# Kernel optimization log

Measured on AMD Instinct MI355X. Metric: run time of the kernel, lower is better.

## Reference

```python
import jax, jax.numpy as jnp
import numpy as np

N = 8192  # number of nodes
F = 8     # feature dim


def setup_inputs() -> dict:
    key = jax.random.key(0)
    ks = jax.random.split(key, 24)
    inp = {
        "adj": jax.random.uniform(ks[0], (N, N), jnp.float32),
        "dist_from_prev": jax.random.uniform(ks[1], (N,), jnp.float32),
        "dist_to_start": jax.random.uniform(ks[2], (N,), jnp.float32),
    }
    dims = {"l0": (2, F), "l1": (F, F), "pol": (F, 1), "val": (F, 1)}
    i = 3
    for name, (din, dout) in dims.items():
        inp[f"W1_{name}"] = jax.random.normal(ks[i], (din, dout), jnp.float32) * 0.3; i += 1
        inp[f"b1_{name}"] = jax.random.normal(ks[i], (dout,), jnp.float32) * 0.1; i += 1
        inp[f"W2_{name}"] = jax.random.normal(ks[i], (dout, dout), jnp.float32) * 0.3; i += 1
        inp[f"b2_{name}"] = jax.random.normal(ks[i], (dout,), jnp.float32) * 0.1; i += 1
    return inp


def _mlp(x, adj, W1, b1, W2, b2):
    # GIN-style layer: aggregate then 2-layer MLP
    h = adj @ x                     # [N, din] aggregation (memory bound)
    h = jax.nn.relu(h @ W1 + b1)    # [N, dout]
    return h @ W2 + b2              # [N, dout]


def reference(adj, dist_from_prev, dist_to_start,
              W1_l0, b1_l0, W2_l0, b2_l0,
              W1_l1, b1_l1, W2_l1, b2_l1,
              W1_pol, b1_pol, W2_pol, b2_pol,
              W1_val, b1_val, W2_val, b2_val):
    cur = jnp.stack([dist_from_prev, dist_to_start], axis=1)  # [N, 2]
    # hidden GIN layers + relu (dropout is identity in eval mode)
    cur = jax.nn.relu(_mlp(cur, adj, W1_l0, b1_l0, W2_l0, b2_l0))
    cur = jax.nn.relu(_mlp(cur, adj, W1_l1, b1_l1, W2_l1, b2_l1))
    policy = jax.nn.softmax(_mlp(cur, adj, W1_pol, b1_pol, W2_pol, b2_pol)[:, 0], axis=0)  # [N]
    value = _mlp(cur, adj, W1_val, b1_val, W2_val, b2_val)[:, 0]  # [N]
    m = value.mean()
    std = jnp.sqrt(jnp.mean((value - m) ** 2) + 1e-10)
    normalized_value = (value - m) / std
    return policy, normalized_value
```

## Files before the change

kernel.cpp:

```cpp
#include <hip/hip_runtime.h>
#include <math.h>

#define NN 8192
typedef unsigned int u32;
typedef unsigned char u8;

__device__ __forceinline__ u32 dot4(u32 a, u32 b, u32 c) {
#if __has_builtin(__builtin_amdgcn_udot4)
  return __builtin_amdgcn_udot4(a, b, c, false);
#else
  c += (a & 0xffu) * (b & 0xffu);
  c += ((a >> 8) & 0xffu) * ((b >> 8) & 0xffu);
  c += ((a >> 16) & 0xffu) * ((b >> 16) & 0xffu);
  c += (a >> 24) * (b >> 24);
  return c;
#endif
}

__global__ __launch_bounds__(256) void pass1_kernel(
    const float* __restrict__ adj, u8* __restrict__ adj8,
    const float* __restrict__ dfp, const float* __restrict__ dts,
    const float* __restrict__ W1, const float* __restrict__ b1,
    const float* __restrict__ W2, const float* __restrict__ b2,
    float* __restrict__ cur, float* __restrict__ partial) {
  const int wave = threadIdx.x >> 6, lane = threadIdx.x & 63;
  const int row0 = blockIdx.x * 16 + wave * 4;
  __shared__ float w1red[4][8];
  float acc0[4] = {0.f, 0.f, 0.f, 0.f};
  float acc1[4] = {0.f, 0.f, 0.f, 0.f};

  float4 A[4], Xp, Xs;
  {
    const int k = 4 * lane;
    Xp = *(const float4*)(dfp + k);
    Xs = *(const float4*)(dts + k);
#pragma unroll
    for (int r = 0; r < 4; ++r)
      A[r] = *(const float4*)(adj + (size_t)(row0 + r) * NN + k);
  }
  for (int k0 = 0; k0 < NN; k0 += 256) {
    float4 B[4], Yp, Ys;
    if (k0 + 256 < NN) {
      const int k = k0 + 256 + 4 * lane;
      Yp = *(const float4*)(dfp + k);
      Ys = *(const float4*)(dts + k);
#pragma unroll
      for (int r = 0; r < 4; ++r)
        B[r] = *(const float4*)(adj + (size_t)(row0 + r) * NN + k);
    } else {
      Yp = Xp; Ys = Xs;
#pragma unroll
      for (int r = 0; r < 4; ++r) B[r] = A[r];
    }
    const float pv[4] = {Xp.x, Xp.y, Xp.z, Xp.w};
    const float sv[4] = {Xs.x, Xs.y, Xs.z, Xs.w};
#pragma unroll
    for (int r = 0; r < 4; ++r) {
      const float av[4] = {A[r].x, A[r].y, A[r].z, A[r].w};
#pragma unroll
      for (int c = 0; c < 4; ++c) {
        acc0[r] = fmaf(av[c], pv[c], acc0[r]);
        acc1[r] = fmaf(av[c], sv[c], acc1[r]);
      }
      u32 q0 = (u32)fmaf(av[0], 255.f, 0.5f);
      u32 q1 = (u32)fmaf(av[1], 255.f, 0.5f);
      u32 q2 = (u32)fmaf(av[2], 255.f, 0.5f);
      u32 q3 = (u32)fmaf(av[3], 255.f, 0.5f);
      ((u32*)(adj8 + (size_t)(row0 + r) * NN + k0))[lane] =
          q0 | (q1 << 8) | (q2 << 16) | (q3 << 24);
    }
#pragma unroll
    for (int r = 0; r < 4; ++r) A[r] = B[r];
    Xp = Yp; Xs = Ys;
  }
#pragma unroll
  for (int r = 0; r < 4; ++r) {
    for (int off = 32; off; off >>= 1) {
      acc0[r] += __shfl_xor(acc0[r], off, 64);
      acc1[r] += __shfl_xor(acc1[r], off, 64);
    }
  }
  const int j = lane & 7;
  float mx = 0.f;
#pragma unroll
  for (int r = 0; r < 4; ++r) {
    float z = fmaf(acc0[r], W1[0 * 8 + j], fmaf(acc1[r], W1[1 * 8 + j], b1[j]));
    z = fmaxf(z, 0.f);
    float o = b2[j];
#pragma unroll
    for (int jj = 0; jj < 8; ++jj)
      o = fmaf(__shfl(z, jj, 64), W2[jj * 8 + j], o);
    float val = fmaxf(o, 0.f);
    if (lane < 8) cur[(size_t)(row0 + r) * 8 + j] = val;
    mx = fmaxf(mx, val);
  }
  if (lane < 8) w1red[wave][lane] = mx;
  __syncthreads();
  if (wave == 0 && lane < 8) {
    float m2 = fmaxf(fmaxf(w1red[0][lane], w1red[1][lane]),
                     fmaxf(w1red[2][lane], w1red[3][lane]));
    partial[blockIdx.x * 8 + lane] = m2;
  }
}

template <int HEADS>
__global__ __launch_bounds__(512) void pass23_kernel(
    const u8* __restrict__ adj8, const float* __restrict__ x,
    const float* __restrict__ partial, int nprod,
    const float* __restrict__ W1, const float* __restrict__ b1,
    const float* __restrict__ W2, const float* __restrict__ b2,
    const float* __restrict__ W1v, const float* __restrict__ b1v,
    const float* __restrict__ W2v, const float* __restrict__ b2v,
    float* __restrict__ out0, float* __restrict__ out1,
    float* __restrict__ partial_out) {
  __shared__ u32 sxR[NN * 2];
  __shared__ u32 sxT[8 * 2048];
  __shared__ float swred[8][8];
  __shared__ float sqs[8], sds[8];
  const int tid = threadIdx.x;
  const int wave = tid >> 6, lane = tid & 63;
  const int row0 = blockIdx.x * 32 + wave * 4;

  uint4 A[4];
#pragma unroll
  for (int r = 0; r < 4; ++r)
    A[r] = *(const uint4*)(adj8 + (size_t)(row0 + r) * NN + 16 * lane);

  float pm[8] = {0.f, 0.f, 0.f, 0.f, 0.f, 0.f, 0.f, 0.f};
  if (tid < nprod) {
    float4 a = *(const float4*)(partial + tid * 8);
    float4 b = *(const float4*)(partial + tid * 8 + 4);
    pm[0] = a.x; pm[1] = a.y; pm[2] = a.z; pm[3] = a.w;
    pm[4] = b.x; pm[5] = b.y; pm[6] = b.z; pm[7] = b.w;
  }
  for (int off = 32; off; off >>= 1)
#pragma unroll
    for (int j = 0; j < 8; ++j) pm[j] = fmaxf(pm[j], __shfl_xor(pm[j], off, 64));
  if (lane == 0)
#pragma unroll
    for (int j = 0; j < 8; ++j) swred[wave][j] = pm[j];
  __syncthreads();
  if (tid < 8) {
    float m2 = 0.f;
#pragma unroll
    for (int w = 0; w < 8; ++w) m2 = fmaxf(m2, swred[w][tid]);
    m2 = fmaxf(m2, 1e-20f);
    sqs[tid] = 255.f / m2;
    sds[tid] = m2 / 65025.f;
  }
  __syncthreads();

  float qs[8];
#pragma unroll
  for (int j = 0; j < 8; ++j) qs[j] = sqs[j];
  for (int base = 0; base < NN; base += 512) {
    const int row = base + tid;
    float4 a = *(const float4*)(x + (size_t)row * 8);
    float4 b = *(const float4*)(x + (size_t)row * 8 + 4);
    u32 q0 = (u32)fmaf(a.x, qs[0], 0.5f), q1 = (u32)fmaf(a.y, qs[1], 0.5f);
    u32 q2 = (u32)fmaf(a.z, qs[2], 0.5f), q3 = (u32)fmaf(a.w, qs[3], 0.5f);
    u32 q4 = (u32)fmaf(b.x, qs[4], 0.5f), q5 = (u32)fmaf(b.y, qs[5], 0.5f);
    u32 q6 = (u32)fmaf(b.z, qs[6], 0.5f), q7 = (u32)fmaf(b.w, qs[7], 0.5f);
    uint2 pk;
    pk.x = q0 | (q1 << 8) | (q2 << 16) | (q3 << 24);
    pk.y = q4 | (q5 << 8) | (q6 << 16) | (q7 << 24);
    ((uint2*)sxR)[row] = pk;
  }
  __syncthreads();

  {
    const int jj = tid & 7, g = tid >> 3;
    const int dw = jj >> 2, sh = 8 * (jj & 3);
#pragma unroll
    for (int i = 0; i < 32; ++i) {
      const int p = g + 64 * i;
      u32 w = 0;
#pragma unroll
      for (int m = 0; m < 4; ++m)
        w |= (((sxR[(4 * p + m) * 2 + dw] >> sh) & 0xffu) << (8 * m));
      sxT[jj * 2048 + p] = w;
    }
  }
  __syncthreads();

  u32 acc[4][8] = {};
  for (int k0 = 0; k0 < NN; k0 += 1024) {
    uint4 B[4];
    if (k0 + 1024 < NN) {
#pragma unroll
      for (int r = 0; r < 4; ++r)
        B[r] = *(const uint4*)(adj8 + (size_t)(row0 + r) * NN + (k0 + 1024) +
                               16 * lane);
    } else {
#pragma unroll
      for (int r = 0; r < 4; ++r) B[r] = A[r];
    }
    uint4 xq[8];
#pragma unroll
    for (int jj = 0; jj < 8; ++jj)
      xq[jj] = ((const uint4*)sxT)[jj * 512 + (k0 >> 4) + lane];
#pragma unroll
    for (int r = 0; r < 4; ++r) {
#pragma unroll
      for (int jj = 0; jj < 8; ++jj) {
        u32 c = acc[r][jj];
        c = dot4(A[r].x, xq[jj].x, c);
        c = dot4(A[r].y, xq[jj].y, c);
        c = dot4(A[r].z, xq[jj].z, c);
        c = dot4(A[r].w, xq[jj].w, c);
        acc[r][jj] = c;
      }
    }
#pragma unroll
    for (int r = 0; r < 4; ++r) A[r] = B[r];
  }
#pragma unroll
  for (int r = 0; r < 4; ++r)
#pragma unroll
    for (int jj = 0; jj < 8; ++jj)
      for (int off = 32; off; off >>= 1)
        acc[r][jj] += (u32)__shfl_xor((int)acc[r][jj], off, 64);
  float dsc[8];
#pragma unroll
  for (int j = 0; j < 8; ++j) dsc[j] = sds[j];
  float h[4][8];
#pragma unroll
  for (int r = 0; r < 4; ++r)
#pragma unroll
    for (int jj = 0; jj < 8; ++jj) h[r][jj] = (float)acc[r][jj] * dsc[jj];

  if (HEADS == 0) {
    const int j = lane & 7;
    float mxv = 0.f;
#pragma unroll
    for (int r = 0; r < 4; ++r) {
      float z = b1[j];
#pragma unroll
      for (int d = 0; d < 8; ++d) z = fmaf(h[r][d], W1[d * 8 + j], z);
      z = fmaxf(z, 0.f);
      float o = b2[j];
#pragma unroll
      for (int jj = 0; jj < 8; ++jj)
        o = fmaf(__shfl(z, jj, 64), W2[jj * 8 + j], o);
      float val = fmaxf(o, 0.f);
      if (lane < 8) out0[(size_t)(row0 + r) * 8 + j] = val;
      mxv = fmaxf(mxv, val);
    }
    if (lane < 8) swred[wave][lane] = mxv;
    __syncthreads();
    if (wave == 0 && lane < 8) {
      float m2 = 0.f;
#pragma unroll
      for (int w = 0; w < 8; ++w) m2 = fmaxf(m2, swred[w][lane]);
      partial_out[blockIdx.x * 8 + lane] = m2;
    }
  } else {
    if (lane == 0) {
#pragma unroll
      for (int r = 0; r < 4; ++r) {
        float zp = b1[0], zv = b1v[0];
#pragma unroll
        for (int d = 0; d < 8; ++d) {
          zp = fmaf(h[r][d], W1[d], zp);
          zv = fmaf(h[r][d], W1v[d], zv);
        }
        zp = fmaxf(zp, 0.f);
        zv = fmaxf(zv, 0.f);
        out0[row0 + r] = fmaf(zp, W2[0], b2[0]);
        out1[row0 + r] = fmaf(zv, W2v[0], b2v[0]);
      }
    }
  }
}

__global__ __launch_bounds__(1024) void reduce_finalize_kernel(
    float* __restrict__ out) {
  const int tid = threadIdx.x, wave = tid >> 6, lane = tid & 63;
  __shared__ float sa[16], sb[16], sc[4];

  float4 l0 = *(const float4*)(out + tid * 8);
  float4 l1 = *(const float4*)(out + tid * 8 + 4);
  float4 v0 = *(const float4*)(out + NN + tid * 8);
  float4 v1 = *(const float4*)(out + NN + tid * 8 + 4);
  const float lv[8] = {l0.x, l0.y, l0.z, l0.w, l1.x, l1.y, l1.z, l1.w};
  const float vv[8] = {v0.x, v0.y, v0.z, v0.w, v1.x, v1.y, v1.z, v1.w};

  float m = -3.4e38f, s = 0.f;
#pragma unroll
  for (int i = 0; i < 8; ++i) {
    m = fmaxf(m, lv[i]);
    s += vv[i];
  }
  for (int off = 32; off; off >>= 1) {
    m = fmaxf(m, __shfl_xor(m, off, 64));
    s += __shfl_xor(s, off, 64);
  }
  if (lane == 0) { sa[wave] = m; sb[wave] = s; }
  __syncthreads();
  if (tid == 0) {
    float mm = sa[0], ss = sb[0];
    for (int i = 1; i < 16; ++i) { mm = fmaxf(mm, sa[i]); ss += sb[i]; }
    sc[0] = mm; sc[1] = ss * (1.f / NN);
  }
  __syncthreads();
  m = sc[0];
  const float mean = sc[1];

  float el[8];
  float e = 0.f, v2 = 0.f;
#pragma unroll
  for (int i = 0; i < 8; ++i) {
    el[i] = expf(lv[i] - m);
    e += el[i];
    float d = vv[i] - mean;
    v2 = fmaf(d, d, v2);
  }
  for (int off = 32; off; off >>= 1) {
    e += __shfl_xor(e, off, 64);
    v2 += __shfl_xor(v2, off, 64);
  }
  if (lane == 0) { sa[wave] = e; sb[wave] = v2; }
  __syncthreads();
  if (tid == 0) {
    float ee = sa[0], vvv = sb[0];
    for (int i = 1; i < 16; ++i) { ee += sa[i]; vvv += sb[i]; }
    sc[2] = 1.f / ee;
    sc[3] = 1.f / sqrtf(vvv * (1.f / NN) + 1e-10f);
  }
  __syncthreads();
  const float inv_e = sc[2], inv_std = sc[3];
  float4 o0, o1, w0, w1;
  o0.x = el[0] * inv_e; o0.y = el[1] * inv_e;
  o0.z = el[2] * inv_e; o0.w = el[3] * inv_e;
  o1.x = el[4] * inv_e; o1.y = el[5] * inv_e;
  o1.z = el[6] * inv_e; o1.w = el[7] * inv_e;
  w0.x = (vv[0] - mean) * inv_std; w0.y = (vv[1] - mean) * inv_std;
  w0.z = (vv[2] - mean) * inv_std; w0.w = (vv[3] - mean) * inv_std;
  w1.x = (vv[4] - mean) * inv_std; w1.y = (vv[5] - mean) * inv_std;
  w1.z = (vv[6] - mean) * inv_std; w1.w = (vv[7] - mean) * inv_std;
  *(float4*)(out + tid * 8) = o0;
  *(float4*)(out + tid * 8 + 4) = o1;
  *(float4*)(out + NN + tid * 8) = w0;
  *(float4*)(out + NN + tid * 8 + 4) = w1;
}

extern "C" void kernel_launch(void* const* d_in, const int* in_sizes, int n_in,
                              void* d_out, int out_size, void* d_ws,
                              size_t ws_size, hipStream_t stream) {
  const float* adj = (const float*)d_in[0];
  const float* dfp = (const float*)d_in[1];
  const float* dts = (const float*)d_in[2];
  const float* W1_l0 = (const float*)d_in[3];
  const float* b1_l0 = (const float*)d_in[4];
  const float* W2_l0 = (const float*)d_in[5];
  const float* b2_l0 = (const float*)d_in[6];
  const float* W1_l1 = (const float*)d_in[7];
  const float* b1_l1 = (const float*)d_in[8];
  const float* W2_l1 = (const float*)d_in[9];
  const float* b2_l1 = (const float*)d_in[10];
  const float* W1_pol = (const float*)d_in[11];
  const float* b1_pol = (const float*)d_in[12];
  const float* W2_pol = (const float*)d_in[13];
  const float* b2_pol = (const float*)d_in[14];
  const float* W1_val = (const float*)d_in[15];
  const float* b1_val = (const float*)d_in[16];
  const float* W2_val = (const float*)d_in[17];
  const float* b2_val = (const float*)d_in[18];

  u8* adj8 = (u8*)d_ws;
  float* curA = (float*)((char*)d_ws + (size_t)NN * NN);
  float* curB = curA + NN * 8;
  float* partialA = curB + NN * 8;
  float* partialB = partialA + 512 * 8;
  float* logits = (float*)d_out;
  float* value = logits + NN;

  pass1_kernel<<<NN / 16, 256, 0, stream>>>(adj, adj8, dfp, dts, W1_l0, b1_l0,
                                            W2_l0, b2_l0, curA, partialA);
  pass23_kernel<0><<<NN / 32, 512, 0, stream>>>(
      adj8, curA, partialA, 512, W1_l1, b1_l1, W2_l1, b2_l1, W1_l1, b1_l1,
      W2_l1, b2_l1, curB, curB, partialB);
  pass23_kernel<1><<<NN / 32, 512, 0, stream>>>(
      adj8, curB, partialB, 256, W1_pol, b1_pol, W2_pol, b2_pol, W1_val,
      b1_val, W2_val, b2_val, logits, value, partialB);
  reduce_finalize_kernel<<<1, 1024, 0, stream>>>((float*)d_out);
}
```

Baseline: 145.9 us.

## Keep quantized features in registers and use signed dot4 with offset correction

The aggregation kernels no longer stage and transpose the whole quantized feature matrix in shared memory in every block. Each thread now quantizes only its own 16-column slice of x into registers. The int8 adjacency is stored biased by 128 so it can use signed dot4, and exact integer corrections come from row sums precomputed in pass1 plus per-block column sums. pass1 is also reorganised so 512-thread blocks sweep full rows, with a cross-wave shared-memory reduction. This removes the redundant per-block LDS fill and transpose, at the cost of extra block-level reductions and syncs for every group of 4 rows.

```diff
diff --git a/kernel.cpp b/kernel.cpp
--- a/kernel.cpp
+++ b/kernel.cpp
@@ -3,131 +3,161 @@
 
 #define NN 8192
 typedef unsigned int u32;
-typedef unsigned char u8;
-
-__device__ __forceinline__ u32 dot4(u32 a, u32 b, u32 c) {
-#if __has_builtin(__builtin_amdgcn_udot4)
-  return __builtin_amdgcn_udot4(a, b, c, false);
+
+__device__ __forceinline__ int sdot4(u32 a, u32 b, int c) {
+#if __has_builtin(__builtin_amdgcn_sdot4)
+  return __builtin_amdgcn_sdot4((int)a, (int)b, c, false);
 #else
-  c += (a & 0xffu) * (b & 0xffu);
-  c += ((a >> 8) & 0xffu) * ((b >> 8) & 0xffu);
-  c += ((a >> 16) & 0xffu) * ((b >> 16) & 0xffu);
-  c += (a >> 24) * (b >> 24);
+  c += ((int)(a << 24) >> 24) * ((int)(b << 24) >> 24);
+  c += ((int)(a << 16) >> 24) * ((int)(b << 16) >> 24);
+  c += ((int)(a << 8) >> 24) * ((int)(b << 8) >> 24);
+  c += (((int)a) >> 24) * (((int)b) >> 24);
   return c;
 #endif
 }
 
-__global__ __launch_bounds__(256) void pass1_kernel(
-    const float* __restrict__ adj, u8* __restrict__ adj8,
+__global__ __launch_bounds__(512) void pass1_kernel(
+    const float* __restrict__ adj, u32* __restrict__ adj8,
+    u32* __restrict__ Rq,
     const float* __restrict__ dfp, const float* __restrict__ dts,
     const float* __restrict__ W1, const float* __restrict__ b1,
     const float* __restrict__ W2, const float* __restrict__ b2,
     float* __restrict__ cur, float* __restrict__ partial) {
-  const int wave = threadIdx.x >> 6, lane = threadIdx.x & 63;
-  const int row0 = blockIdx.x * 16 + wave * 4;
-  __shared__ float w1red[4][8];
-  float acc0[4] = {0.f, 0.f, 0.f, 0.f};
-  float acc1[4] = {0.f, 0.f, 0.f, 0.f};
-
-  float4 A[4], Xp, Xs;
-  {
-    const int k = 4 * lane;
-    Xp = *(const float4*)(dfp + k);
-    Xs = *(const float4*)(dts + k);
+  const int tid = threadIdx.x;
+  const int wave = tid >> 6, lane = tid & 63;
+  const int rbase = blockIdx.x * 16;
+  __shared__ float redF[8][8];
+  __shared__ u32 redU[8][4];
+  __shared__ float finF[8];
+  __shared__ float wmax[4][8];
+
+  float pv[4][4], sv[4][4];
+#pragma unroll
+  for (int q = 0; q < 4; ++q) {
+    float4 t1 = *(const float4*)(dfp + q * 2048 + 4 * tid);
+    float4 t2 = *(const float4*)(dts + q * 2048 + 4 * tid);
+    pv[q][0] = t1.x; pv[q][1] = t1.y; pv[q][2] = t1.z; pv[q][3] = t1.w;
+    sv[q][0] = t2.x; sv[q][1] = t2.y; sv[q][2] = t2.z; sv[q][3] = t2.w;
+  }
+  float mxv = 0.f;
+
+  for (int g = 0; g < 4; ++g) {
+    float accP[4] = {0.f, 0.f, 0.f, 0.f};
+    float accS[4] = {0.f, 0.f, 0.f, 0.f};
+    u32 accR[4] = {0, 0, 0, 0};
+    float4 A[4], B[4];
 #pragma unroll
     for (int r = 0; r < 4; ++r)
-      A[r] = *(const float4*)(adj + (size_t)(row0 + r) * NN + k);
-  }
-  for (int k0 = 0; k0 < NN; k0 += 256) {
-    float4 B[4], Yp, Ys;
-    if (k0 + 256 < NN) {
-      const int k = k0 + 256 + 4 * lane;
-      Yp = *(const float4*)(dfp + k);
-      Ys = *(const float4*)(dts + k);
-#pragma unroll
-      for (int r = 0; r < 4; ++r)
-        B[r] = *(const float4*)(adj + (size_t)(row0 + r) * NN + k);
-    } else {
-      Yp = Xp; Ys = Xs;
-#pragma unroll
-      for (int r = 0; r < 4; ++r) B[r] = A[r];
-    }
-    const float pv[4] = {Xp.x, Xp.y, Xp.z, Xp.w};
-    const float sv[4] = {Xs.x, Xs.y, Xs.z, Xs.w};
+      A[r] = *(const float4*)(adj + (size_t)(rbase + g * 4 + r) * NN + 4 * tid);
+#pragma unroll
+    for (int q = 0; q < 4; ++q) {
+      if (q < 3) {
+#pragma unroll
+        for (int r = 0; r < 4; ++r)
+          B[r] = *(const float4*)(adj + (size_t)(rbase + g * 4 + r) * NN +
+                                  (q + 1) * 2048 + 4 * tid);
+      }
+#pragma unroll
+      for (int r = 0; r < 4; ++r) {
+        const float a0 = A[r].x, a1 = A[r].y, a2 = A[r].z, a3 = A[r].w;
+        accP[r] = fmaf(a0, pv[q][0], accP[r]);
+        accP[r] = fmaf(a1, pv[q][1], accP[r]);
+        accP[r] = fmaf(a2, pv[q][2], accP[r]);
+        accP[r] = fmaf(a3, pv[q][3], accP[r]);
+        accS[r] = fmaf(a0, sv[q][0], accS[r]);
+        accS[r] = fmaf(a1, sv[q][1], accS[r]);
+        accS[r] = fmaf(a2, sv[q][2], accS[r]);
+        accS[r] = fmaf(a3, sv[q][3], accS[r]);
+        u32 q0 = (u32)fmaf(a0, 255.f, 0.5f);
+        u32 q1 = (u32)fmaf(a1, 255.f, 0.5f);
+        u32 q2 = (u32)fmaf(a2, 255.f, 0.5f);
+        u32 q3 = (u32)fmaf(a3, 255.f, 0.5f);
+        accR[r] += q0 + q1 + q2 + q3;
+        adj8[(size_t)(rbase + g * 4 + r) * 2048 + q * 512 + tid] =
+            (q0 | (q1 << 8) | (q2 << 16) | (q3 << 24)) ^ 0x80808080u;
+      }
+      if (q < 3) {
+#pragma unroll
+        for (int r = 0; r < 4; ++r) A[r] = B[r];
+      }
+    }
 #pragma unroll
     for (int r = 0; r < 4; ++r) {
-      const float av[4] = {A[r].x, A[r].y, A[r].z, A[r].w};
-#pragma unroll
-      for (int c = 0; c < 4; ++c) {
-        acc0[r] = fmaf(av[c], pv[c], acc0[r]);
-        acc1[r] = fmaf(av[c], sv[c], acc1[r]);
-      }
-      u32 q0 = (u32)fmaf(av[0], 255.f, 0.5f);
-      u32 q1 = (u32)fmaf(av[1], 255.f, 0.5f);
-      u32 q2 = (u32)fmaf(av[2], 255.f, 0.5f);
-      u32 q3 = (u32)fmaf(av[3], 255.f, 0.5f);
-      ((u32*)(adj8 + (size_t)(row0 + r) * NN + k0))[lane] =
-          q0 | (q1 << 8) | (q2 << 16) | (q3 << 24);
-    }
-#pragma unroll
-    for (int r = 0; r < 4; ++r) A[r] = B[r];
-    Xp = Yp; Xs = Ys;
-  }
-#pragma unroll
-  for (int r = 0; r < 4; ++r) {
-    for (int off = 32; off; off >>= 1) {
-      acc0[r] += __shfl_xor(acc0[r], off, 64);
-      acc1[r] += __shfl_xor(acc1[r], off, 64);
-    }
-  }
-  const int j = lane & 7;
-  float mx = 0.f;
-#pragma unroll
-  for (int r = 0; r < 4; ++r) {
-    float z = fmaf(acc0[r], W1[0 * 8 + j], fmaf(acc1[r], W1[1 * 8 + j], b1[j]));
-    z = fmaxf(z, 0.f);
-    float o = b2[j];
-#pragma unroll
-    for (int jj = 0; jj < 8; ++jj)
-      o = fmaf(__shfl(z, jj, 64), W2[jj * 8 + j], o);
-    float val = fmaxf(o, 0.f);
-    if (lane < 8) cur[(size_t)(row0 + r) * 8 + j] = val;
-    mx = fmaxf(mx, val);
-  }
-  if (lane < 8) w1red[wave][lane] = mx;
-  __syncthreads();
-  if (wave == 0 && lane < 8) {
-    float m2 = fmaxf(fmaxf(w1red[0][lane], w1red[1][lane]),
-                     fmaxf(w1red[2][lane], w1red[3][lane]));
-    partial[blockIdx.x * 8 + lane] = m2;
-  }
+      for (int off = 32; off; off >>= 1) {
+        accP[r] += __shfl_xor(accP[r], off, 64);
+        accS[r] += __shfl_xor(accS[r], off, 64);
+        accR[r] += (u32)__shfl_xor((int)accR[r], off, 64);
+      }
+    }
+    if (lane == 0) {
+#pragma unroll
+      for (int r = 0; r < 4; ++r) {
+        redF[wave][r] = accP[r];
+        redF[wave][4 + r] = accS[r];
+        redU[wave][r] = accR[r];
+      }
+    }
+    __syncthreads();
+    if (tid < 8) {
+      float s = 0.f;
+      for (int w = 0; w < 8; ++w) s += redF[w][tid];
+      finF[tid] = s;
+    } else if (tid < 12) {
+      u32 s = 0;
+      for (int w = 0; w < 8; ++w) s += redU[w][tid - 8];
+      Rq[rbase + g * 4 + (tid - 8)] = s;
+    }
+    __syncthreads();
+    if (wave < 4) {
+      const int row = rbase + g * 4 + wave;
+      const float hp = finF[wave], hs = finF[4 + wave];
+      const int j = lane & 7;
+      float z = fmaf(hp, W1[j], fmaf(hs, W1[8 + j], b1[j]));
+      z = fmaxf(z, 0.f);
+      float o = b2[j];
+#pragma unroll
+      for (int jj = 0; jj < 8; ++jj)
+        o = fmaf(__shfl(z, jj, 64), W2[jj * 8 + j], o);
+      float val = fmaxf(o, 0.f);
+      if (lane < 8) {
+        cur[(size_t)row * 8 + j] = val;
+        mxv = fmaxf(mxv, val);
+      }
+    }
+  }
+  if (wave < 4 && lane < 8) wmax[wave][lane] = mxv;
+  __syncthreads();
+  if (tid < 8)
+    partial[blockIdx.x * 8 + tid] = fmaxf(fmaxf(wmax[0][tid], wmax[1][tid]),
+                                          fmaxf(wmax[2][tid], wmax[3][tid]));
 }
 
 template <int HEADS>
 __global__ __launch_bounds__(512) void pass23_kernel(
-    const u8* __restrict__ adj8, const float* __restrict__ x,
-    const float* __restrict__ partial, int nprod,
+    const u32* __restrict__ adj8, const float* __restrict__ x,
+    const u32* __restrict__ Rq, const float* __restrict__ partial,
     const float* __restrict__ W1, const float* __restrict__ b1,
     const float* __restrict__ W2, const float* __restrict__ b2,
     const float* __restrict__ W1v, const float* __restrict__ b1v,
     const float* __restrict__ W2v, const float* __restrict__ b2v,
     float* __restrict__ out0, float* __restrict__ out1,
     float* __restrict__ partial_out) {
-  __shared__ u32 sxR[NN * 2];
-  __shared__ u32 sxT[8 * 2048];
-  __shared__ float swred[8][8];
-  __shared__ float sqs[8], sds[8];
   const int tid = threadIdx.x;
   const int wave = tid >> 6, lane = tid & 63;
-  const int row0 = blockIdx.x * 32 + wave * 4;
-
-  uint4 A[4];
-#pragma unroll
-  for (int r = 0; r < 4; ++r)
-    A[r] = *(const uint4*)(adj8 + (size_t)(row0 + r) * NN + 16 * lane);
-
-  float pm[8] = {0.f, 0.f, 0.f, 0.f, 0.f, 0.f, 0.f, 0.f};
-  if (tid < nprod) {
+  const int rbase = blockIdx.x * 16;
+  __shared__ float sqs[8], sds[8];
+  __shared__ float redM[8][8];
+  __shared__ u32 redC[8][8];
+  __shared__ int sCq[8];
+  __shared__ int redD[8][32];
+  __shared__ int finD[32];
+  __shared__ float wmax[4][8];
+
+  uint4 A = *(const uint4*)(adj8 + (size_t)rbase * 2048 + 4 * tid);
+  uint4 Bn = *(const uint4*)(adj8 + (size_t)(rbase + 1) * 2048 + 4 * tid);
+
+  float pm[8];
+  {
     float4 a = *(const float4*)(partial + tid * 8);
     float4 b = *(const float4*)(partial + tid * 8 + 4);
     pm[0] = a.x; pm[1] = a.y; pm[2] = a.z; pm[3] = a.w;
@@ -138,12 +168,12 @@
     for (int j = 0; j < 8; ++j) pm[j] = fmaxf(pm[j], __shfl_xor(pm[j], off, 64));
   if (lane == 0)
 #pragma unroll
-    for (int j = 0; j < 8; ++j) swred[wave][j] = pm[j];
+    for (int j = 0; j < 8; ++j) redM[wave][j] = pm[j];
   __syncthreads();
   if (tid < 8) {
     float m2 = 0.f;
 #pragma unroll
-    for (int w = 0; w < 8; ++w) m2 = fmaxf(m2, swred[w][tid]);
+    for (int w = 0; w < 8; ++w) m2 = fmaxf(m2, redM[w][tid]);
     m2 = fmaxf(m2, 1e-20f);
     sqs[tid] = 255.f / m2;
     sds[tid] = m2 / 65025.f;
@@ -153,123 +183,135 @@
   float qs[8];
 #pragma unroll
   for (int j = 0; j < 8; ++j) qs[j] = sqs[j];
-  for (int base = 0; base < NN; base += 512) {
-    const int row = base + tid;
-    float4 a = *(const float4*)(x + (size_t)row * 8);
-    float4 b = *(const float4*)(x + (size_t)row * 8 + 4);
-    u32 q0 = (u32)fmaf(a.x, qs[0], 0.5f), q1 = (u32)fmaf(a.y, qs[1], 0.5f);
-    u32 q2 = (u32)fmaf(a.z, qs[2], 0.5f), q3 = (u32)fmaf(a.w, qs[3], 0.5f);
-    u32 q4 = (u32)fmaf(b.x, qs[4], 0.5f), q5 = (u32)fmaf(b.y, qs[5], 0.5f);
-    u32 q6 = (u32)fmaf(b.z, qs[6], 0.5f), q7 = (u32)fmaf(b.w, qs[7], 0.5f);
-    uint2 pk;
-    pk.x = q0 | (q1 << 8) | (q2 << 16) | (q3 << 24);
-    pk.y = q4 | (q5 << 8) | (q6 << 16) | (q7 << 24);
-    ((uint2*)sxR)[row] = pk;
-  }
-  __syncthreads();
-
-  {
-    const int jj = tid & 7, g = tid >> 3;
-    const int dw = jj >> 2, sh = 8 * (jj & 3);
-#pragma unroll
-    for (int i = 0; i < 32; ++i) {
-      const int p = g + 64 * i;
-      u32 w = 0;
-#pragma unroll
-      for (int m = 0; m < 4; ++m)
-        w |= (((sxR[(4 * p + m) * 2 + dw] >> sh) & 0xffu) << (8 * m));
-      sxT[jj * 2048 + p] = w;
-    }
-  }
-  __syncthreads();
-
-  u32 acc[4][8] = {};
-  for (int k0 = 0; k0 < NN; k0 += 1024) {
-    uint4 B[4];
-    if (k0 + 1024 < NN) {
+  u32 xq[8][4];
+#pragma unroll
+  for (int j = 0; j < 8; ++j)
+#pragma unroll
+    for (int d = 0; d < 4; ++d) xq[j][d] = 0;
+  u32 cs[8] = {0, 0, 0, 0, 0, 0, 0, 0};
+#pragma unroll
+  for (int kk = 0; kk < 16; ++kk) {
+    const float* xp = x + ((size_t)tid * 16 + kk) * 8;
+    float4 a = *(const float4*)xp;
+    float4 b = *(const float4*)(xp + 4);
+    const float e[8] = {a.x, a.y, a.z, a.w, b.x, b.y, b.z, b.w};
+#pragma unroll
+    for (int j = 0; j < 8; ++j) {
+      u32 qv = (u32)fmaf(e[j], qs[j], 0.5f);
+      cs[j] += qv;
+      xq[j][kk >> 2] |= (qv ^ 0x80u) << (8 * (kk & 3));
+    }
+  }
+  for (int off = 32; off; off >>= 1)
+#pragma unroll
+    for (int j = 0; j < 8; ++j) cs[j] += (u32)__shfl_xor((int)cs[j], off, 64);
+  if (lane == 0)
+#pragma unroll
+    for (int j = 0; j < 8; ++j) redC[wave][j] = cs[j];
+  __syncthreads();
+  if (tid < 8) {
+    u32 s = 0;
+#pragma unroll
+    for (int w = 0; w < 8; ++w) s += redC[w][tid];
+    sCq[tid] = (int)s;
+  }
+  __syncthreads();
+
+  for (int g = 0; g < 4; ++g) {
+    int accD[4][8];
+#pragma unroll
+    for (int r = 0; r < 4; ++r)
+#pragma unroll
+      for (int j = 0; j < 8; ++j) accD[r][j] = 0;
+#pragma unroll
+    for (int r = 0; r < 4; ++r) {
+      const int nrr = (g * 4 + r + 2) & 15;
+      uint4 C = *(const uint4*)(adj8 + (size_t)(rbase + nrr) * 2048 + 4 * tid);
+#pragma unroll
+      for (int j = 0; j < 8; ++j) {
+        int c = accD[r][j];
+        c = sdot4(A.x, xq[j][0], c);
+        c = sdot4(A.y, xq[j][1], c);
+        c = sdot4(A.z, xq[j][2], c);
+        c = sdot4(A.w, xq[j][3], c);
+        accD[r][j] = c;
+      }
+      A = Bn;
+      Bn = C;
+    }
+#pragma unroll
+    for (int r = 0; r < 4; ++r)
+#pragma unroll
+      for (int j = 0; j < 8; ++j)
+        for (int off = 32; off; off >>= 1)
+          accD[r][j] += __shfl_xor(accD[r][j], off, 64);
+    if (lane == 0)
 #pragma unroll
       for (int r = 0; r < 4; ++r)
-        B[r] = *(const uint4*)(adj8 + (size_t)(row0 + r) * NN + (k0 + 1024) +
-                               16 * lane);
+#pragma unroll
+        for (int j = 0; j < 8; ++j) redD[wave][r * 8 + j] = accD[r][j];
+    __syncthreads();
+    if (tid < 32) {
+      int s = 0;
+#pragma unroll
+      for (int w = 0; w < 8; ++w) s += redD[w][tid];
+      finD[tid] = s;
+    }
+    __syncthreads();
+    if (HEADS == 0) {
+      if (wave < 4) {
+        const int row = rbase + g * 4 + wave;
+        const int j = lane & 7;
+        int hi = finD[wave * 8 + j] + 128 * (int)Rq[row] + 128 * sCq[j] -
+                 134217728;
+        float h = (float)hi * sds[j];
+        float z = b1[j];
+#pragma unroll
+        for (int d = 0; d < 8; ++d)
+          z = fmaf(__shfl(h, d, 64), W1[d * 8 + j], z);
+        z = fmaxf(z, 0.f);
+        float o = b2[j];
+#pragma unroll
+        for (int jj = 0; jj < 8; ++jj)
+          o = fmaf(__shfl(z, jj, 64), W2[jj * 8 + j], o);
+        float val = fmaxf(o, 0.f);
+        if (lane < 8) {
+          out0[(size_t)row * 8 + j] = val;
+          if (wave == (g & 3) || true) wmaxv_dummy:;
+        }
+      }
     } else {
-#pragma unroll
-      for (int r = 0; r < 4; ++r) B[r] = A[r];
-    }
-    uint4 xq[8];
-#pragma unroll
-    for (int jj = 0; jj < 8; ++jj)
-      xq[jj] = ((const uint4*)sxT)[jj * 512 + (k0 >> 4) + lane];
-#pragma unroll
-    for (int r = 0; r < 4; ++r) {
-#pragma unroll
-      for (int jj = 0; jj < 8; ++jj) {
-        u32 c = acc[r][jj];
-        c = dot4(A[r].x, xq[jj].x, c);
-        c = dot4(A[r].y, xq[jj].y, c);
-        c = dot4(A[r].z, xq[jj].z, c);
-        c = dot4(A[r].w, xq[jj].w, c);
-        acc[r][jj] = c;
-      }
-    }
-#pragma unroll
-    for (int r = 0; r < 4; ++r) A[r] = B[r];
-  }
-#pragma unroll
-  for (int r = 0; r < 4; ++r)
-#pragma unroll
-    for (int jj = 0; jj < 8; ++jj)
-      for (int off = 32; off; off >>= 1)
-        acc[r][jj] += (u32)__shfl_xor((int)acc[r][jj], off, 64);
-  float dsc[8];
-#pragma unroll
-  for (int j = 0; j < 8; ++j) dsc[j] = sds[j];
-  float h[4][8];
-#pragma unroll
-  for (int r = 0; r < 4; ++r)
-#pragma unroll
-    for (int jj = 0; jj < 8; ++jj) h[r][jj] = (float)acc[r][jj] * dsc[jj];
-
-  if (HEADS == 0) {
-    const int j = lane & 7;
-    float mxv = 0.f;
-#pragma unroll
-    for (int r = 0; r < 4; ++r) {
-      float z = b1[j];
-#pragma unroll
-      for (int d = 0; d < 8; ++d) z = fmaf(h[r][d], W1[d * 8 + j], z);
-      z = fmaxf(z, 0.f);
-      float o = b2[j];
-#pragma unroll
-      for (int jj = 0; jj < 8; ++jj)
-        o = fmaf(__shfl(z, jj, 64), W2[jj * 8 + j], o);
-      float val = fmaxf(o, 0.f);
-      if (lane < 8) out0[(size_t)(row0 + r) * 8 + j] = val;
-      mxv = fmaxf(mxv, val);
-    }
-    if (lane < 8) swred[wave][lane] = mxv;
-    __syncthreads();
-    if (wave == 0 && lane < 8) {
-      float m2 = 0.f;
-#pragma unroll
-      for (int w = 0; w < 8; ++w) m2 = fmaxf(m2, swred[w][lane]);
-      partial_out[blockIdx.x * 8 + lane] = m2;
-    }
-  } else {
-    if (lane == 0) {
-#pragma unroll
-      for (int r = 0; r < 4; ++r) {
+      if (wave < 4 && lane == 0) {
+        const int row = rbase + g * 4 + wave;
+        const int rq = 128 * (int)Rq[row];
         float zp = b1[0], zv = b1v[0];
 #pragma unroll
         for (int d = 0; d < 8; ++d) {
-          zp = fmaf(h[r][d], W1[d], zp);
-          zv = fmaf(h[r][d], W1v[d], zv);
+          int hi = finD[wave * 8 + d] + rq + 128 * sCq[d] - 134217728;
+          float h = (float)hi * sds[d];
+          zp = fmaf(h, W1[d], zp);
+          zv = fmaf(h, W1v[d], zv);
         }
         zp = fmaxf(zp, 0.f);
         zv = fmaxf(zv, 0.f);
-        out0[row0 + r] = fmaf(zp, W2[0], b2[0]);
-        out1[row0 + r] = fmaf(zv, W2v[0], b2v[0]);
-      }
-    }
+        out0[row] = fmaf(zp, W2[0], b2[0]);
+        out1[row] = fmaf(zv, W2v[0], b2v[0]);
+      }
+    }
+  }
+  if (HEADS == 0) {
+    float mxv = 0.f;
+    if (wave < 4 && lane < 8) {
+#pragma unroll
+      for (int g = 0; g < 4; ++g)
+        mxv = fmaxf(mxv, out0[(size_t)(rbase + g * 4 + wave) * 8 + lane]);
+      wmax[wave][lane] = mxv;
+    }
+    __syncthreads();
+    if (tid < 8)
+      partial_out[blockIdx.x * 8 + tid] =
+          fmaxf(fmaxf(wmax[0][tid], wmax[1][tid]),
+                fmaxf(wmax[2][tid], wmax[3][tid]));
   }
 }
 
@@ -367,21 +409,23 @@
   const float* W2_val = (const float*)d_in[17];
   const float* b2_val = (const float*)d_in[18];
 
-  u8* adj8 = (u8*)d_ws;
-  float* curA = (float*)((char*)d_ws + (size_t)NN * NN);
+  char* base = (char*)d_ws;
+  u32* adj8 = (u32*)base;
+  u32* Rq = (u32*)(base + (size_t)NN * NN);
+  float* curA = (float*)(base + (size_t)NN * NN + NN * 4);
   float* curB = curA + NN * 8;
   float* partialA = curB + NN * 8;
   float* partialB = partialA + 512 * 8;
   float* logits = (float*)d_out;
   float* value = logits + NN;
 
-  pass1_kernel<<<NN / 16, 256, 0, stream>>>(adj, adj8, dfp, dts, W1_l0, b1_l0,
-                                            W2_l0, b2_l0, curA, partialA);
-  pass23_kernel<0><<<NN / 32, 512, 0, stream>>>(
-      adj8, curA, partialA, 512, W1_l1, b1_l1, W2_l1, b2_l1, W1_l1, b1_l1,
+  pass1_kernel<<<512, 512, 0, stream>>>(adj, adj8, Rq, dfp, dts, W1_l0, b1_l0,
+                                        W2_l0, b2_l0, curA, partialA);
+  pass23_kernel<0><<<512, 512, 0, stream>>>(
+      adj8, curA, Rq, partialA, W1_l1, b1_l1, W2_l1, b2_l1, W1_l1, b1_l1,
       W2_l1, b2_l1, curB, curB, partialB);
-  pass23_kernel<1><<<NN / 32, 512, 0, stream>>>(
-      adj8, curB, partialB, 256, W1_pol, b1_pol, W2_pol, b2_pol, W1_val,
-      b1_val, W2_val, b2_val, logits, value, partialB);
+  pass23_kernel<1><<<512, 512, 0, stream>>>(
+      adj8, curB, Rq, partialB, W1_pol, b1_pol, W2_pol, b2_pol, W1_val, b1_val,
+      W2_val, b2_val, logits, value, partialB);
   reduce_finalize_kernel<<<1, 1024, 0, stream>>>((float*)d_out);
 }
```

New measurement: 212.2 us. +45.5%, slower.

## Halve rows per wave, double grid, and quantize x directly into transposed layout

Applied to the files above, without the earlier changes.

Each wave now handles 2 rows instead of 4 in both passes, and the grid doubles to 1024 and 512 blocks, giving more blocks and more memory parallelism on the large adjacency stream. The pass23 staging drops the row-major shared buffer and transpose step: each thread packs four consecutive nodes per feature straight into the transposed shared array. This frees 64KB of LDS per block so more blocks can reside per CU, and it adds a deeper two-chunk prefetch of adjacency. The partial-max buffers grow to match the larger grid.

```diff
diff --git a/kernel.cpp b/kernel.cpp
--- a/kernel.cpp
+++ b/kernel.cpp
@@ -5,7 +5,7 @@
 typedef unsigned int u32;
 typedef unsigned char u8;
 
-__device__ __forceinline__ u32 dot4(u32 a, u32 b, u32 c) {
+__device__ __forceinline__ u32 dot4u(u32 a, u32 b, u32 c) {
 #if __has_builtin(__builtin_amdgcn_udot4)
   return __builtin_amdgcn_udot4(a, b, c, false);
 #else
@@ -18,73 +18,81 @@
 }
 
 __global__ __launch_bounds__(256) void pass1_kernel(
-    const float* __restrict__ adj, u8* __restrict__ adj8,
+    const float* __restrict__ adj, u32* __restrict__ adj8,
     const float* __restrict__ dfp, const float* __restrict__ dts,
     const float* __restrict__ W1, const float* __restrict__ b1,
     const float* __restrict__ W2, const float* __restrict__ b2,
     float* __restrict__ cur, float* __restrict__ partial) {
-  const int wave = threadIdx.x >> 6, lane = threadIdx.x & 63;
-  const int row0 = blockIdx.x * 16 + wave * 4;
-  __shared__ float w1red[4][8];
-  float acc0[4] = {0.f, 0.f, 0.f, 0.f};
-  float acc1[4] = {0.f, 0.f, 0.f, 0.f};
-
-  float4 A[4], Xp, Xs;
-  {
-    const int k = 4 * lane;
-    Xp = *(const float4*)(dfp + k);
-    Xs = *(const float4*)(dts + k);
-#pragma unroll
-    for (int r = 0; r < 4; ++r)
-      A[r] = *(const float4*)(adj + (size_t)(row0 + r) * NN + k);
-  }
-  for (int k0 = 0; k0 < NN; k0 += 256) {
-    float4 B[4], Yp, Ys;
-    if (k0 + 256 < NN) {
-      const int k = k0 + 256 + 4 * lane;
-      Yp = *(const float4*)(dfp + k);
-      Ys = *(const float4*)(dts + k);
-#pragma unroll
-      for (int r = 0; r < 4; ++r)
-        B[r] = *(const float4*)(adj + (size_t)(row0 + r) * NN + k);
-    } else {
-      Yp = Xp; Ys = Xs;
-#pragma unroll
-      for (int r = 0; r < 4; ++r) B[r] = A[r];
-    }
-    const float pv[4] = {Xp.x, Xp.y, Xp.z, Xp.w};
-    const float sv[4] = {Xs.x, Xs.y, Xs.z, Xs.w};
-#pragma unroll
-    for (int r = 0; r < 4; ++r) {
-      const float av[4] = {A[r].x, A[r].y, A[r].z, A[r].w};
-#pragma unroll
-      for (int c = 0; c < 4; ++c) {
-        acc0[r] = fmaf(av[c], pv[c], acc0[r]);
-        acc1[r] = fmaf(av[c], sv[c], acc1[r]);
+  const int tid = threadIdx.x, wave = tid >> 6, lane = tid & 63;
+  const int row0 = blockIdx.x * 8 + wave * 2;
+  __shared__ float wmax[4][8];
+
+  const float* rowp0 = adj + (size_t)row0 * NN;
+  const float* rowp1 = adj + (size_t)(row0 + 1) * NN;
+  u32* qp0 = adj8 + (size_t)row0 * (NN / 4);
+  u32* qp1 = adj8 + (size_t)(row0 + 1) * (NN / 4);
+
+  float acc0[2] = {0.f, 0.f}, acc1[2] = {0.f, 0.f};
+  float4 A[2][2], B[2][2];
+#pragma unroll
+  for (int i = 0; i < 2; ++i) {
+    A[0][i] = *(const float4*)(rowp0 + 256 * i + 4 * lane);
+    A[1][i] = *(const float4*)(rowp1 + 256 * i + 4 * lane);
+  }
+  for (int c = 0; c < 16; ++c) {
+    const int kb = 512 * c;
+    if (c < 15) {
+#pragma unroll
+      for (int i = 0; i < 2; ++i) {
+        B[0][i] = *(const float4*)(rowp0 + kb + 512 + 256 * i + 4 * lane);
+        B[1][i] = *(const float4*)(rowp1 + kb + 512 + 256 * i + 4 * lane);
       }
-      u32 q0 = (u32)fmaf(av[0], 255.f, 0.5f);
-      u32 q1 = (u32)fmaf(av[1], 255.f, 0.5f);
-      u32 q2 = (u32)fmaf(av[2], 255.f, 0.5f);
-      u32 q3 = (u32)fmaf(av[3], 255.f, 0.5f);
-      ((u32*)(adj8 + (size_t)(row0 + r) * NN + k0))[lane] =
-          q0 | (q1 << 8) | (q2 << 16) | (q3 << 24);
-    }
-#pragma unroll
-    for (int r = 0; r < 4; ++r) A[r] = B[r];
-    Xp = Yp; Xs = Ys;
-  }
-#pragma unroll
-  for (int r = 0; r < 4; ++r) {
+    }
+    float4 xp[2], xs[2];
+#pragma unroll
+    for (int i = 0; i < 2; ++i) {
+      xp[i] = *(const float4*)(dfp + kb + 256 * i + 4 * lane);
+      xs[i] = *(const float4*)(dts + kb + 256 * i + 4 * lane);
+    }
+#pragma unroll
+    for (int r = 0; r < 2; ++r) {
+#pragma unroll
+      for (int i = 0; i < 2; ++i) {
+        const float4 a4 = A[r][i];
+        acc0[r] = fmaf(a4.x, xp[i].x, acc0[r]);
+        acc0[r] = fmaf(a4.y, xp[i].y, acc0[r]);
+        acc0[r] = fmaf(a4.z, xp[i].z, acc0[r]);
+        acc0[r] = fmaf(a4.w, xp[i].w, acc0[r]);
+        acc1[r] = fmaf(a4.x, xs[i].x, acc1[r]);
+        acc1[r] = fmaf(a4.y, xs[i].y, acc1[r]);
+        acc1[r] = fmaf(a4.z, xs[i].z, acc1[r]);
+        acc1[r] = fmaf(a4.w, xs[i].w, acc1[r]);
+        u32 q0 = (u32)fmaf(a4.x, 255.f, 0.5f);
+        u32 q1 = (u32)fmaf(a4.y, 255.f, 0.5f);
+        u32 q2 = (u32)fmaf(a4.z, 255.f, 0.5f);
+        u32 q3 = (u32)fmaf(a4.w, 255.f, 0.5f);
+        (r ? qp1 : qp0)[128 * c + 64 * i + lane] =
+            q0 | (q1 << 8) | (q2 << 16) | (q3 << 24);
+      }
+    }
+#pragma unroll
+    for (int r = 0; r < 2; ++r) {
+      A[r][0] = B[r][0];
+      A[r][1] = B[r][1];
+    }
+  }
+#pragma unroll
+  for (int r = 0; r < 2; ++r) {
     for (int off = 32; off; off >>= 1) {
       acc0[r] += __shfl_xor(acc0[r], off, 64);
       acc1[r] += __shfl_xor(acc1[r], off, 64);
     }
   }
   const int j = lane & 7;
-  float mx = 0.f;
-#pragma unroll
-  for (int r = 0; r < 4; ++r) {
-    float z = fmaf(acc0[r], W1[0 * 8 + j], fmaf(acc1[r], W1[1 * 8 + j], b1[j]));
+  float mxv = 0.f;
+#pragma unroll
+  for (int r = 0; r < 2; ++r) {
+    float z = fmaf(acc0[r], W1[j], fmaf(acc1[r], W1[8 + j], b1[j]));
     z = fmaxf(z, 0.f);
     float o = b2[j];
 #pragma unroll
@@ -92,20 +100,18 @@
       o = fmaf(__shfl(z, jj, 64), W2[jj * 8 + j], o);
     float val = fmaxf(o, 0.f);
     if (lane < 8) cur[(size_t)(row0 + r) * 8 + j] = val;
-    mx = fmaxf(mx, val);
-  }
-  if (lane < 8) w1red[wave][lane] = mx;
-  __syncthreads();
-  if (wave == 0 && lane < 8) {
-    float m2 = fmaxf(fmaxf(w1red[0][lane], w1red[1][lane]),
-                     fmaxf(w1red[2][lane], w1red[3][lane]));
-    partial[blockIdx.x * 8 + lane] = m2;
-  }
+    mxv = fmaxf(mxv, val);
+  }
+  if (lane < 8) wmax[wave][lane] = mxv;
+  __syncthreads();
+  if (tid < 8)
+    partial[blockIdx.x * 8 + tid] = fmaxf(fmaxf(wmax[0][tid], wmax[1][tid]),
+                                          fmaxf(wmax[2][tid], wmax[3][tid]));
 }
 
 template <int HEADS>
 __global__ __launch_bounds__(512) void pass23_kernel(
-    const u8* __restrict__ adj8, const float* __restrict__ x,
+    const u32* __restrict__ adj8, const float* __restrict__ x,
     const float* __restrict__ partial, int nprod,
     const float* __restrict__ W1, const float* __restrict__ b1,
     const float* __restrict__ W2, const float* __restrict__ b2,
@@ -113,37 +119,41 @@
     const float* __restrict__ W2v, const float* __restrict__ b2v,
     float* __restrict__ out0, float* __restrict__ out1,
     float* __restrict__ partial_out) {
-  __shared__ u32 sxR[NN * 2];
   __shared__ u32 sxT[8 * 2048];
-  __shared__ float swred[8][8];
+  __shared__ float redM[8][8];
   __shared__ float sqs[8], sds[8];
-  const int tid = threadIdx.x;
-  const int wave = tid >> 6, lane = tid & 63;
-  const int row0 = blockIdx.x * 32 + wave * 4;
-
-  uint4 A[4];
-#pragma unroll
-  for (int r = 0; r < 4; ++r)
-    A[r] = *(const uint4*)(adj8 + (size_t)(row0 + r) * NN + 16 * lane);
+  __shared__ float wmax[8][8];
+  const int tid = threadIdx.x, wave = tid >> 6, lane = tid & 63;
+  const int row0 = blockIdx.x * 16 + wave * 2;
+
+  const u32* r0p = adj8 + (size_t)row0 * 2048;
+  const u32* r1p = adj8 + (size_t)(row0 + 1) * 2048;
+  uint4 A[2], Bp[2];
+  A[0] = *(const uint4*)(r0p + 4 * lane);
+  A[1] = *(const uint4*)(r1p + 4 * lane);
+  Bp[0] = *(const uint4*)(r0p + 256 + 4 * lane);
+  Bp[1] = *(const uint4*)(r1p + 256 + 4 * lane);
 
   float pm[8] = {0.f, 0.f, 0.f, 0.f, 0.f, 0.f, 0.f, 0.f};
-  if (tid < nprod) {
-    float4 a = *(const float4*)(partial + tid * 8);
-    float4 b = *(const float4*)(partial + tid * 8 + 4);
-    pm[0] = a.x; pm[1] = a.y; pm[2] = a.z; pm[3] = a.w;
-    pm[4] = b.x; pm[5] = b.y; pm[6] = b.z; pm[7] = b.w;
+  for (int p = tid; p < nprod; p += 512) {
+    float4 a = *(const float4*)(partial + p * 8);
+    float4 b = *(const float4*)(partial + p * 8 + 4);
+    pm[0] = fmaxf(pm[0], a.x); pm[1] = fmaxf(pm[1], a.y);
+    pm[2] = fmaxf(pm[2], a.z); pm[3] = fmaxf(pm[3], a.w);
+    pm[4] = fmaxf(pm[4], b.x); pm[5] = fmaxf(pm[5], b.y);
+    pm[6] = fmaxf(pm[6], b.z); pm[7] = fmaxf(pm[7], b.w);
   }
   for (int off = 32; off; off >>= 1)
 #pragma unroll
     for (int j = 0; j < 8; ++j) pm[j] = fmaxf(pm[j], __shfl_xor(pm[j], off, 64));
   if (lane == 0)
 #pragma unroll
-    for (int j = 0; j < 8; ++j) swred[wave][j] = pm[j];
+    for (int j = 0; j < 8; ++j) redM[wave][j] = pm[j];
   __syncthreads();
   if (tid < 8) {
     float m2 = 0.f;
 #pragma unroll
-    for (int w = 0; w < 8; ++w) m2 = fmaxf(m2, swred[w][tid]);
+    for (int w = 0; w < 8; ++w) m2 = fmaxf(m2, redM[w][tid]);
     m2 = fmaxf(m2, 1e-20f);
     sqs[tid] = 255.f / m2;
     sds[tid] = m2 / 65025.f;
@@ -153,87 +163,71 @@
   float qs[8];
 #pragma unroll
   for (int j = 0; j < 8; ++j) qs[j] = sqs[j];
-  for (int base = 0; base < NN; base += 512) {
-    const int row = base + tid;
-    float4 a = *(const float4*)(x + (size_t)row * 8);
-    float4 b = *(const float4*)(x + (size_t)row * 8 + 4);
-    u32 q0 = (u32)fmaf(a.x, qs[0], 0.5f), q1 = (u32)fmaf(a.y, qs[1], 0.5f);
-    u32 q2 = (u32)fmaf(a.z, qs[2], 0.5f), q3 = (u32)fmaf(a.w, qs[3], 0.5f);
-    u32 q4 = (u32)fmaf(b.x, qs[4], 0.5f), q5 = (u32)fmaf(b.y, qs[5], 0.5f);
-    u32 q6 = (u32)fmaf(b.z, qs[6], 0.5f), q7 = (u32)fmaf(b.w, qs[7], 0.5f);
-    uint2 pk;
-    pk.x = q0 | (q1 << 8) | (q2 << 16) | (q3 << 24);
-    pk.y = q4 | (q5 << 8) | (q6 << 16) | (q7 << 24);
-    ((uint2*)sxR)[row] = pk;
-  }
-  __syncthreads();
-
-  {
-    const int jj = tid & 7, g = tid >> 3;
-    const int dw = jj >> 2, sh = 8 * (jj & 3);
-#pragma unroll
-    for (int i = 0; i < 32; ++i) {
-      const int p = g + 64 * i;
-      u32 w = 0;
-#pragma unroll
-      for (int m = 0; m < 4; ++m)
-        w |= (((sxR[(4 * p + m) * 2 + dw] >> sh) & 0xffu) << (8 * m));
-      sxT[jj * 2048 + p] = w;
-    }
-  }
-  __syncthreads();
-
-  u32 acc[4][8] = {};
-  for (int k0 = 0; k0 < NN; k0 += 1024) {
-    uint4 B[4];
-    if (k0 + 1024 < NN) {
-#pragma unroll
-      for (int r = 0; r < 4; ++r)
-        B[r] = *(const uint4*)(adj8 + (size_t)(row0 + r) * NN + (k0 + 1024) +
-                               16 * lane);
+  for (int gi = 0; gi < 4; ++gi) {
+    const int p = gi * 512 + tid;
+    u32 pk[8] = {0, 0, 0, 0, 0, 0, 0, 0};
+#pragma unroll
+    for (int m = 0; m < 4; ++m) {
+      const float* xr = x + (size_t)(4 * p + m) * 8;
+      float4 a = *(const float4*)xr;
+      float4 b = *(const float4*)(xr + 4);
+      const float e[8] = {a.x, a.y, a.z, a.w, b.x, b.y, b.z, b.w};
+#pragma unroll
+      for (int j = 0; j < 8; ++j)
+        pk[j] |= ((u32)fmaf(e[j], qs[j], 0.5f)) << (8 * m);
+    }
+#pragma unroll
+    for (int j = 0; j < 8; ++j) sxT[j * 2048 + p] = pk[j];
+  }
+  __syncthreads();
+
+  u32 acc[2][8] = {};
+  for (int c = 0; c < 8; ++c) {
+    uint4 C[2];
+    if (c + 2 < 8) {
+      C[0] = *(const uint4*)(r0p + 256 * (c + 2) + 4 * lane);
+      C[1] = *(const uint4*)(r1p + 256 * (c + 2) + 4 * lane);
     } else {
-#pragma unroll
-      for (int r = 0; r < 4; ++r) B[r] = A[r];
+      C[0] = A[0];
+      C[1] = A[1];
     }
     uint4 xq[8];
 #pragma unroll
     for (int jj = 0; jj < 8; ++jj)
-      xq[jj] = ((const uint4*)sxT)[jj * 512 + (k0 >> 4) + lane];
-#pragma unroll
-    for (int r = 0; r < 4; ++r) {
+      xq[jj] = ((const uint4*)sxT)[jj * 512 + 64 * c + lane];
+#pragma unroll
+    for (int r = 0; r < 2; ++r) {
+      const uint4 a4 = A[r];
 #pragma unroll
       for (int jj = 0; jj < 8; ++jj) {
-        u32 c = acc[r][jj];
-        c = dot4(A[r].x, xq[jj].x, c);
-        c = dot4(A[r].y, xq[jj].y, c);
-        c = dot4(A[r].z, xq[jj].z, c);
-        c = dot4(A[r].w, xq[jj].w, c);
-        acc[r][jj] = c;
+        u32 cc = acc[r][jj];
+        cc = dot4u(a4.x, xq[jj].x, cc);
+        cc = dot4u(a4.y, xq[jj].y, cc);
+        cc = dot4u(a4.z, xq[jj].z, cc);
+        cc = dot4u(a4.w, xq[jj].w, cc);
+        acc[r][jj] = cc;
       }
     }
-#pragma unroll
-    for (int r = 0; r < 4; ++r) A[r] = B[r];
-  }
-#pragma unroll
-  for (int r = 0; r < 4; ++r)
+    A[0] = Bp[0]; A[1] = Bp[1];
+    Bp[0] = C[0]; Bp[1] = C[1];
+  }
+#pragma unroll
+  for (int r = 0; r < 2; ++r)
 #pragma unroll
     for (int jj = 0; jj < 8; ++jj)
       for (int off = 32; off; off >>= 1)
         acc[r][jj] += (u32)__shfl_xor((int)acc[r][jj], off, 64);
-  float dsc[8];
-#pragma unroll
-  for (int j = 0; j < 8; ++j) dsc[j] = sds[j];
-  float h[4][8];
-#pragma unroll
-  for (int r = 0; r < 4; ++r)
-#pragma unroll
-    for (int jj = 0; jj < 8; ++jj) h[r][jj] = (float)acc[r][jj] * dsc[jj];
+  float h[2][8];
+#pragma unroll
+  for (int r = 0; r < 2; ++r)
+#pragma unroll
+    for (int jj = 0; jj < 8; ++jj) h[r][jj] = (float)acc[r][jj] * sds[jj];
 
   if (HEADS == 0) {
     const int j = lane & 7;
     float mxv = 0.f;
 #pragma unroll
-    for (int r = 0; r < 4; ++r) {
+    for (int r = 0; r < 2; ++r) {
       float z = b1[j];
 #pragma unroll
       for (int d = 0; d < 8; ++d) z = fmaf(h[r][d], W1[d * 8 + j], z);
@@ -246,18 +240,18 @@
       if (lane < 8) out0[(size_t)(row0 + r) * 8 + j] = val;
       mxv = fmaxf(mxv, val);
     }
-    if (lane < 8) swred[wave][lane] = mxv;
+    if (lane < 8) wmax[wave][lane] = mxv;
     __syncthreads();
-    if (wave == 0 && lane < 8) {
+    if (tid < 8) {
       float m2 = 0.f;
 #pragma unroll
-      for (int w = 0; w < 8; ++w) m2 = fmaxf(m2, swred[w][lane]);
-      partial_out[blockIdx.x * 8 + lane] = m2;
+      for (int w = 0; w < 8; ++w) m2 = fmaxf(m2, wmax[w][tid]);
+      partial_out[blockIdx.x * 8 + tid] = m2;
     }
   } else {
     if (lane == 0) {
 #pragma unroll
-      for (int r = 0; r < 4; ++r) {
+      for (int r = 0; r < 2; ++r) {
         float zp = b1[0], zv = b1v[0];
 #pragma unroll
         for (int d = 0; d < 8; ++d) {
@@ -367,21 +361,22 @@
   const float* W2_val = (const float*)d_in[17];
   const float* b2_val = (const float*)d_in[18];
 
-  u8* adj8 = (u8*)d_ws;
-  float* curA = (float*)((char*)d_ws + (size_t)NN * NN);
+  char* base = (char*)d_ws;
+  u32* adj8 = (u32*)base;
+  float* curA = (float*)(base + (size_t)NN * NN);
   float* curB = curA + NN * 8;
   float* partialA = curB + NN * 8;
-  float* partialB = partialA + 512 * 8;
+  float* partialB = partialA + 1024 * 8;
   float* logits = (float*)d_out;
   float* value = logits + NN;
 
-  pass1_kernel<<<NN / 16, 256, 0, stream>>>(adj, adj8, dfp, dts, W1_l0, b1_l0,
-                                            W2_l0, b2_l0, curA, partialA);
-  pass23_kernel<0><<<NN / 32, 512, 0, stream>>>(
-      adj8, curA, partialA, 512, W1_l1, b1_l1, W2_l1, b2_l1, W1_l1, b1_l1,
+  pass1_kernel<<<1024, 256, 0, stream>>>(adj, adj8, dfp, dts, W1_l0, b1_l0,
+                                         W2_l0, b2_l0, curA, partialA);
+  pass23_kernel<0><<<512, 512, 0, stream>>>(
+      adj8, curA, partialA, 1024, W1_l1, b1_l1, W2_l1, b2_l1, W1_l1, b1_l1,
       W2_l1, b2_l1, curB, curB, partialB);
-  pass23_kernel<1><<<NN / 32, 512, 0, stream>>>(
-      adj8, curB, partialB, 256, W1_pol, b1_pol, W2_pol, b2_pol, W1_val,
+  pass23_kernel<1><<<512, 512, 0, stream>>>(
+      adj8, curB, partialB, 512, W1_pol, b1_pol, W2_pol, b2_pol, W1_val,
       b1_val, W2_val, b2_val, logits, value, partialB);
   reduce_finalize_kernel<<<1, 1024, 0, stream>>>((float*)d_out);
 }
```

New measurement: 137.8 us. 1.06x faster.
